# Kernel tuning notes

Measured on AMD Instinct MI355X. Metric: run time of the kernel, lower is better.

Reference implementation:

```python
import jax, jax.numpy as jnp
import numpy as np

N = 50000
E = 800000
IN_C = 1024
HID = 64
HEADS = 4
OUT_C = 64
NEG_SLOPE = 0.2  # PyG GATConv default


def setup_inputs() -> dict:
    key = jax.random.key(0)
    ks = jax.random.split(key, 12)
    x = jax.random.normal(ks[0], (N, IN_C), dtype=jnp.float32)
    edge_index = jax.random.randint(ks[1], (2, E), 0, N, dtype=jnp.int64)
    s1 = 1.0 / np.sqrt(IN_C)
    s2 = 1.0 / np.sqrt(HEADS * HID)
    return {
        "x": x,
        "edge_index": edge_index,
        "W1": jax.random.normal(ks[2], (HEADS * HID, IN_C), dtype=jnp.float32) * s1,
        "a_src1": jax.random.normal(ks[3], (HEADS, HID), dtype=jnp.float32) * s2,
        "a_dst1": jax.random.normal(ks[4], (HEADS, HID), dtype=jnp.float32) * s2,
        "b1": jnp.zeros((HEADS * HID,), dtype=jnp.float32),
        "W2": jax.random.normal(ks[5], (OUT_C, HEADS * HID), dtype=jnp.float32) * s2,
        "a_src2": jax.random.normal(ks[6], (1, OUT_C), dtype=jnp.float32) * 0.1,
        "a_dst2": jax.random.normal(ks[7], (1, OUT_C), dtype=jnp.float32) * 0.1,
        "b2": jnp.zeros((OUT_C,), dtype=jnp.float32),
    }


def gat_conv(x, src, dst, W, a_src, a_dst, b, heads, concat):
    # x: [N, F_in]; src/dst: [E'] (self-loops already appended)
    n = x.shape[0]
    h = (x @ W.T).reshape(n, heads, -1)                 # [N, H, C]
    alpha_s = (h * a_src).sum(-1)                       # [N, H]
    alpha_d = (h * a_dst).sum(-1)                       # [N, H]
    e = jax.nn.leaky_relu(alpha_s[src] + alpha_d[dst], NEG_SLOPE)  # [E', H]
    # segment softmax over edges grouped by destination
    m = jax.ops.segment_max(e, dst, num_segments=n)     # [N, H]
    ex = jnp.exp(e - m[dst])
    denom = jax.ops.segment_sum(ex, dst, num_segments=n)
    alpha = ex / denom[dst]                             # [E', H]
    out = jax.ops.segment_sum(alpha[:, :, None] * h[src], dst, num_segments=n)  # [N, H, C]
    out = out.reshape(n, -1) if concat else out.mean(axis=1)
    return out + b


def reference(x, edge_index, W1, a_src1, a_dst1, b1, W2, a_src2, a_dst2, b2):
    n = x.shape[0]
    loop = jnp.arange(n, dtype=edge_index.dtype)
    src = jnp.concatenate([edge_index[0], loop])  # PyG add_self_loops=True
    dst = jnp.concatenate([edge_index[1], loop])
    # eval mode: dropout is identity
    h = gat_conv(x, src, dst, W1, a_src1, a_dst1, b1, HEADS, concat=True)
    h = jax.nn.elu(h)
    out = gat_conv(h, src, dst, W2, a_src2, a_dst2, b2, 1, concat=False)
    return out
```

## Files before the change

kernel.cpp:

```cpp
#include <hip/hip_runtime.h>
#include <hip/hip_bf16.h>
#include <math.h>

constexpr int IN_C = 1024;
constexpr int HEADS = 4;
constexpr int F1 = 256;
constexpr int OUT_C = 64;
constexpr float NEG = 0.2f;

using bf16x8 = __attribute__((ext_vector_type(8))) short;
using f32x4 = __attribute__((ext_vector_type(4))) float;

__device__ __forceinline__ float leaky(float x) { return x > 0.f ? x : NEG * x; }

__device__ __forceinline__ unsigned short bf16bits(float v) {
  __hip_bfloat16 b = __float2bfloat16(v);
  return *reinterpret_cast<unsigned short*>(&b);
}
__device__ __forceinline__ float bf2f(unsigned short u) {
  union { unsigned u; float f; } c; c.u = (unsigned)u << 16; return c.f;
}

#define GLD_LDS16(g, l)                                                        \
  __builtin_amdgcn_global_load_lds(                                            \
      (const __attribute__((address_space(1))) void*)(g),                      \
      (__attribute__((address_space(3))) void*)(l), 16, 0, 0)

constexpr int NB_W1 = (F1 * IN_C) / 256;
constexpr int NB_W2 = (OUT_C * F1) / 256;

__global__ __launch_bounds__(256) void prep_kernel(const float* __restrict__ W1,
                                                   unsigned short* __restrict__ W1b,
                                                   const float* __restrict__ W2,
                                                   unsigned short* __restrict__ W2b,
                                                   const int* __restrict__ ei, int E, int N,
                                                   int* __restrict__ deg) {
  int b = blockIdx.x;
  if (b < NB_W1) {
    int i = b * 256 + threadIdx.x;
    W1b[i] = bf16bits(W1[i]);
  } else if (b < NB_W1 + NB_W2) {
    int i = (b - NB_W1) * 256 + threadIdx.x;
    W2b[i] = bf16bits(W2[i]);
  } else {
    int e = (b - NB_W1 - NB_W2) * 256 + threadIdx.x;
    if (e < E + N) {
      int dst = (e < E) ? ei[E + e] : (e - E);
      atomicAdd(&deg[dst], 1);
    }
  }
}

constexpr int LDTA = 72;

__global__ __launch_bounds__(256, 3) void gemm1_mfma(const float* __restrict__ X,
                                                     const unsigned short* __restrict__ Wb,
                                                     unsigned short* __restrict__ Hb,
                                                     const float* __restrict__ a_src,
                                                     const float* __restrict__ a_dst,
                                                     float* __restrict__ as_out,
                                                     float* __restrict__ ad_out, int M, int MB,
                                                     const int* __restrict__ ei, int E, int N,
                                                     const int* __restrict__ row_ptr,
                                                     int* __restrict__ fill,
                                                     int* __restrict__ col) {
  __shared__ unsigned short As[64 * LDTA];
  __shared__ unsigned short Bs[256 * 64];
  const int tid = threadIdx.x;

  if (blockIdx.x >= MB) {
    int e = (blockIdx.x - MB) * 256 + tid;
    int ET = E + N;
    if (e < ET) {
      int src, dst;
      if (e < E) { src = ei[e]; dst = ei[E + e]; }
      else       { src = e - E; dst = e - E; }
      int pos = row_ptr[dst] + atomicAdd(&fill[dst], 1);
      col[pos] = src;
    }
    return;
  }

  const int wave = tid >> 6;
  const int lane = tid & 63;
  const int m15 = lane & 15;
  const int q = lane >> 4;
  const int bm = blockIdx.x * 64;

  f32x4 acc[4][4];
#pragma unroll
  for (int i = 0; i < 4; ++i)
#pragma unroll
    for (int j = 0; j < 4; ++j) acc[i][j] = (f32x4){0.f, 0.f, 0.f, 0.f};

  const int ar = tid >> 2;
  const int acg = (tid & 3) * 16;
  const int agr = (bm + ar < M) ? (bm + ar) : (M - 1);
  const float* aptr = X + (size_t)agr * IN_C + acg;

  float4 a0 = *(const float4*)(aptr + 0);
  float4 a1 = *(const float4*)(aptr + 4);
  float4 a2 = *(const float4*)(aptr + 8);
  float4 a3 = *(const float4*)(aptr + 12);

  for (int kt = 0; kt < IN_C; kt += 64) {
#pragma unroll
    for (int p = 0; p < 8; ++p) {
      int s = p * 256 + tid;
      int r = s >> 3;
      int cb = s & 7;
      const unsigned short* g = Wb + (size_t)r * IN_C + kt + ((cb ^ (r & 7)) << 3);
      GLD_LDS16(g, &Bs[(p * 256 + wave * 64) * 8]);
    }
    union { uint4 u4[2]; __hip_bfloat162 h[8]; } pk;
    pk.h[0] = __float22bfloat162_rn(make_float2(a0.x, a0.y));
    pk.h[1] = __float22bfloat162_rn(make_float2(a0.z, a0.w));
    pk.h[2] = __float22bfloat162_rn(make_float2(a1.x, a1.y));
    pk.h[3] = __float22bfloat162_rn(make_float2(a1.z, a1.w));
    pk.h[4] = __float22bfloat162_rn(make_float2(a2.x, a2.y));
    pk.h[5] = __float22bfloat162_rn(make_float2(a2.z, a2.w));
    pk.h[6] = __float22bfloat162_rn(make_float2(a3.x, a3.y));
    pk.h[7] = __float22bfloat162_rn(make_float2(a3.z, a3.w));
    *(uint4*)&As[ar * LDTA + acg] = pk.u4[0];
    *(uint4*)&As[ar * LDTA + acg + 8] = pk.u4[1];
    if (kt + 64 < IN_C) {
      a0 = *(const float4*)(aptr + kt + 64 + 0);
      a1 = *(const float4*)(aptr + kt + 64 + 4);
      a2 = *(const float4*)(aptr + kt + 64 + 8);
      a3 = *(const float4*)(aptr + kt + 64 + 12);
    }
    __syncthreads();

#pragma unroll
    for (int k0 = 0; k0 < 64; k0 += 32) {
      bf16x8 af[4], bfr[4];
#pragma unroll
      for (int i = 0; i < 4; ++i)
        af[i] = *(const bf16x8*)&As[(i * 16 + m15) * LDTA + k0 + q * 8];
#pragma unroll
      for (int j = 0; j < 4; ++j) {
        int rb = wave * 64 + j * 16 + m15;
        int cbp = ((k0 >> 3) + q) ^ (rb & 7);
        bfr[j] = *(const bf16x8*)&Bs[rb * 64 + cbp * 8];
      }
#pragma unroll
      for (int i = 0; i < 4; ++i)
#pragma unroll
        for (int j = 0; j < 4; ++j)
          acc[i][j] = __builtin_amdgcn_mfma_f32_16x16x32_bf16(af[i], bfr[j], acc[i][j], 0, 0, 0);
    }
    __syncthreads();
  }
  float asf[4], adf[4];
#pragma unroll
  for (int j = 0; j < 4; ++j) {
    asf[j] = a_src[wave * 64 + j * 16 + m15];
    adf[j] = a_dst[wave * 64 + j * 16 + m15];
  }
#pragma unroll
  for (int i = 0; i < 4; ++i) {
#pragma unroll
    for (int r = 0; r < 4; ++r) {
      int row = bm + i * 16 + q * 4 + r;
      if (row < M) {
#pragma unroll
        for (int j = 0; j < 4; ++j)
          Hb[(size_t)row * F1 + wave * 64 + j * 16 + m15] = bf16bits(acc[i][j][r]);
      }
      float s = acc[i][0][r] * asf[0] + acc[i][1][r] * asf[1] +
                acc[i][2][r] * asf[2] + acc[i][3][r] * asf[3];
      float d = acc[i][0][r] * adf[0] + acc[i][1][r] * adf[1] +
                acc[i][2][r] * adf[2] + acc[i][3][r] * adf[3];
#pragma unroll
      for (int o = 1; o < 16; o <<= 1) {
        s += __shfl_xor(s, o, 64);
        d += __shfl_xor(d, o, 64);
      }
      if (m15 == 0 && row < M) {
        as_out[row * HEADS + wave] = s;
        ad_out[row * HEADS + wave] = d;
      }
    }
  }
}

__global__ __launch_bounds__(256, 4) void gemm2_mfma(const unsigned short* __restrict__ Y,
                                                     const unsigned short* __restrict__ W2b,
                                                     float* __restrict__ H2,
                                                     const float* __restrict__ a_src,
                                                     const float* __restrict__ a_dst,
                                                     float* __restrict__ as_out,
                                                     float* __restrict__ ad_out, int M) {
  __shared__ unsigned short As[64 * 64];
  __shared__ unsigned short Bs[64 * 64];
  const int tid = threadIdx.x;
  const int wave = tid >> 6;
  const int lane = tid & 63;
  const int m15 = lane & 15;
  const int q = lane >> 4;
  const int bm = blockIdx.x * 64;

  f32x4 acc[4];
#pragma unroll
  for (int j = 0; j < 4; ++j) acc[j] = (f32x4){0.f, 0.f, 0.f, 0.f};

  for (int kt = 0; kt < F1; kt += 64) {
#pragma unroll
    for (int p = 0; p < 2; ++p) {
      int s = p * 256 + tid;
      int r = s >> 3;
      int cb = s & 7;
      int colo = (cb ^ (r & 7)) << 3;
      int gr = (bm + r < M) ? (bm + r) : (M - 1);
      GLD_LDS16(Y + (size_t)gr * F1 + kt + colo, &As[(p * 256 + wave * 64) * 8]);
      GLD_LDS16(W2b + (size_t)r * F1 + kt + colo, &Bs[(p * 256 + wave * 64) * 8]);
    }
    __syncthreads();
#pragma unroll
    for (int k0 = 0; k0 < 64; k0 += 32) {
      int ra = wave * 16 + m15;
      bf16x8 af = *(const bf16x8*)&As[ra * 64 + ((((k0 >> 3) + q) ^ (ra & 7)) << 3)];
      bf16x8 bfr[4];
#pragma unroll
      for (int j = 0; j < 4; ++j) {
        int rb = j * 16 + m15;
        bfr[j] = *(const bf16x8*)&Bs[rb * 64 + ((((k0 >> 3) + q) ^ (rb & 7)) << 3)];
      }
#pragma unroll
      for (int j = 0; j < 4; ++j)
        acc[j] = __builtin_amdgcn_mfma_f32_16x16x32_bf16(af, bfr[j], acc[j], 0, 0, 0);
    }
    __syncthreads();
  }
  float asf[4], adf[4];
#pragma unroll
  for (int j = 0; j < 4; ++j) {
    asf[j] = a_src[j * 16 + m15];
    adf[j] = a_dst[j * 16 + m15];
  }
#pragma unroll
  for (int r = 0; r < 4; ++r) {
    int row = bm + wave * 16 + q * 4 + r;
    if (row < M) {
#pragma unroll
      for (int j = 0; j < 4; ++j) H2[(size_t)row * OUT_C + j * 16 + m15] = acc[j][r];
    }
    float s = acc[0][r] * asf[0] + acc[1][r] * asf[1] + acc[2][r] * asf[2] + acc[3][r] * asf[3];
    float d = acc[0][r] * adf[0] + acc[1][r] * adf[1] + acc[2][r] * adf[2] + acc[3][r] * adf[3];
#pragma unroll
    for (int o = 1; o < 16; o <<= 1) {
      s += __shfl_xor(s, o, 64);
      d += __shfl_xor(d, o, 64);
    }
    if (m15 == 0 && row < M) {
      as_out[row] = s;
      ad_out[row] = d;
    }
  }
}

__global__ __launch_bounds__(256) void scan_block_sums(const int* __restrict__ deg,
                                                       int* __restrict__ part, int n) {
  __shared__ int sm[256];
  int t = threadIdx.x;
  int i = blockIdx.x * 256 + t;
  sm[t] = (i < n) ? deg[i] : 0;
  __syncthreads();
  for (int off = 128; off > 0; off >>= 1) {
    if (t < off) sm[t] += sm[t + off];
    __syncthreads();
  }
  if (t == 0) part[blockIdx.x] = sm[0];
}

__global__ __launch_bounds__(256) void scan_final2(const int* __restrict__ deg,
                                                   const int* __restrict__ part,
                                                   int* __restrict__ row_ptr, int n) {
  __shared__ int sm[256];
  __shared__ int wsum[4];
  int t = threadIdx.x;
  int i = blockIdx.x * 256 + t;
  sm[t] = (i < n) ? deg[i] : 0;
  int pv = (t < blockIdx.x) ? part[t] : 0;
#pragma unroll
  for (int o = 1; o < 64; o <<= 1) pv += __shfl_xor(pv, o, 64);
  if ((t & 63) == 0) wsum[t >> 6] = pv;
  __syncthreads();
  for (int off = 1; off < 256; off <<= 1) {
    int u = (t >= off) ? sm[t - off] : 0;
    __syncthreads();
    sm[t] += u;
    __syncthreads();
  }
  int base = wsum[0] + wsum[1] + wsum[2] + wsum[3];
  if (i < n) row_ptr[i + 1] = base + sm[t];
  if (i == 0) row_ptr[0] = 0;
}

__global__ __launch_bounds__(256) void agg1_kernel(const unsigned short* __restrict__ hb,
                                                   const float* __restrict__ as,
                                                   const float* __restrict__ ad,
                                                   const int* __restrict__ row_ptr,
                                                   const int* __restrict__ col,
                                                   const float* __restrict__ bias,
                                                   unsigned short* __restrict__ yb, int N) {
  int dst = (blockIdx.x * blockDim.x + threadIdx.x) >> 6;
  int lane = threadIdx.x & 63;
  if (dst >= N) return;
  const int s0 = row_ptr[dst], s1 = row_ptr[dst + 1];
  const int par = lane >> 5;
  const int cg = lane & 31;
  const int hh = cg >> 3;
  const float adl = ad[dst * 4 + hh];
  float acc[8];
#pragma unroll
  for (int k = 0; k < 8; ++k) acc[k] = 0.f;
  float den = 0.f;

  int i = s0 + par;
  for (; i + 6 < s1; i += 8) {
    int sA = col[i], sB = col[i + 2], sC = col[i + 4], sD = col[i + 6];
    float wA = __expf(leaky(as[sA * 4 + hh] + adl));
    float wB = __expf(leaky(as[sB * 4 + hh] + adl));
    float wC = __expf(leaky(as[sC * 4 + hh] + adl));
    float wD = __expf(leaky(as[sD * 4 + hh] + adl));
    uint4 hA = *(const uint4*)(hb + (size_t)sA * F1 + cg * 8);
    uint4 hB = *(const uint4*)(hb + (size_t)sB * F1 + cg * 8);
    uint4 hC = *(const uint4*)(hb + (size_t)sC * F1 + cg * 8);
    uint4 hD = *(const uint4*)(hb + (size_t)sD * F1 + cg * 8);
    den += (wA + wB) + (wC + wD);
    const unsigned short* pa = (const unsigned short*)&hA;
    const unsigned short* pb = (const unsigned short*)&hB;
    const unsigned short* pc = (const unsigned short*)&hC;
    const unsigned short* pd = (const unsigned short*)&hD;
#pragma unroll
    for (int k = 0; k < 8; ++k) {
      acc[k] = fmaf(wA, bf2f(pa[k]), acc[k]);
      acc[k] = fmaf(wB, bf2f(pb[k]), acc[k]);
      acc[k] = fmaf(wC, bf2f(pc[k]), acc[k]);
      acc[k] = fmaf(wD, bf2f(pd[k]), acc[k]);
    }
  }
  for (; i + 2 < s1; i += 4) {
    int sA = col[i], sB = col[i + 2];
    float wA = __expf(leaky(as[sA * 4 + hh] + adl));
    float wB = __expf(leaky(as[sB * 4 + hh] + adl));
    uint4 hA = *(const uint4*)(hb + (size_t)sA * F1 + cg * 8);
    uint4 hB = *(const uint4*)(hb + (size_t)sB * F1 + cg * 8);
    den += wA + wB;
    const unsigned short* pa = (const unsigned short*)&hA;
    const unsigned short* pb = (const unsigned short*)&hB;
#pragma unroll
    for (int k = 0; k < 8; ++k) {
      acc[k] = fmaf(wA, bf2f(pa[k]), acc[k]);
      acc[k] = fmaf(wB, bf2f(pb[k]), acc[k]);
    }
  }
  for (; i < s1; i += 2) {
    int s = col[i];
    float w = __expf(leaky(as[s * 4 + hh] + adl));
    uint4 hv = *(const uint4*)(hb + (size_t)s * F1 + cg * 8);
    den += w;
    const unsigned short* p = (const unsigned short*)&hv;
#pragma unroll
    for (int k = 0; k < 8; ++k) acc[k] = fmaf(w, bf2f(p[k]), acc[k]);
  }
  den += __shfl_xor(den, 32, 64);
#pragma unroll
  for (int k = 0; k < 8; ++k) acc[k] += __shfl_xor(acc[k], 32, 64);

  if (par == 0) {
    const float iv = 1.f / den;
    float4 b0 = *(const float4*)(bias + cg * 8);
    float4 b1 = *(const float4*)(bias + cg * 8 + 4);
    float bv[8] = {b0.x, b0.y, b0.z, b0.w, b1.x, b1.y, b1.z, b1.w};
    ushort4 o[2];
    unsigned short* po = (unsigned short*)o;
#pragma unroll
    for (int k = 0; k < 8; ++k) {
      float v = acc[k] * iv + bv[k];
      v = v > 0.f ? v : (__expf(v) - 1.f);
      po[k] = bf16bits(v);
    }
    *(uint4*)(yb + (size_t)dst * F1 + cg * 8) = *(uint4*)o;
  }
}

__global__ __launch_bounds__(256) void agg2_kernel(const float* __restrict__ h,
                                                   const float* __restrict__ as,
                                                   const float* __restrict__ ad,
                                                   const int* __restrict__ row_ptr,
                                                   const int* __restrict__ col,
                                                   const float* __restrict__ bias,
                                                   float* __restrict__ out, int N) {
  int dst = (blockIdx.x * blockDim.x + threadIdx.x) >> 6;
  int lane = threadIdx.x & 63;
  if (dst >= N) return;
  const int s0 = row_ptr[dst], s1 = row_ptr[dst + 1];
  const int par = lane >> 5;
  const int cg = lane & 31;
  const float adl = ad[dst];
  float a0 = 0.f, a1 = 0.f, den = 0.f;

  int i = s0 + par;
  for (; i + 6 < s1; i += 8) {
    int sA = col[i], sB = col[i + 2], sC = col[i + 4], sD = col[i + 6];
    float wA = __expf(leaky(as[sA] + adl));
    float wB = __expf(leaky(as[sB] + adl));
    float wC = __expf(leaky(as[sC] + adl));
    float wD = __expf(leaky(as[sD] + adl));
    float2 hA = *(const float2*)(h + (size_t)sA * OUT_C + cg * 2);
    float2 hB = *(const float2*)(h + (size_t)sB * OUT_C + cg * 2);
    float2 hC = *(const float2*)(h + (size_t)sC * OUT_C + cg * 2);
    float2 hD = *(const float2*)(h + (size_t)sD * OUT_C + cg * 2);
    den += (wA + wB) + (wC + wD);
    a0 = fmaf(wA, hA.x, a0); a1 = fmaf(wA, hA.y, a1);
    a0 = fmaf(wB, hB.x, a0); a1 = fmaf(wB, hB.y, a1);
    a0 = fmaf(wC, hC.x, a0); a1 = fmaf(wC, hC.y, a1);
    a0 = fmaf(wD, hD.x, a0); a1 = fmaf(wD, hD.y, a1);
  }
  for (; i + 2 < s1; i += 4) {
    int sA = col[i], sB = col[i + 2];
    float wA = __expf(leaky(as[sA] + adl));
    float wB = __expf(leaky(as[sB] + adl));
    float2 hA = *(const float2*)(h + (size_t)sA * OUT_C + cg * 2);
    float2 hB = *(const float2*)(h + (size_t)sB * OUT_C + cg * 2);
    den += wA + wB;
    a0 = fmaf(wA, hA.x, a0); a1 = fmaf(wA, hA.y, a1);
    a0 = fmaf(wB, hB.x, a0); a1 = fmaf(wB, hB.y, a1);
  }
  for (; i < s1; i += 2) {
    int s = col[i];
    float w = __expf(leaky(as[s] + adl));
    float2 hv = *(const float2*)(h + (size_t)s * OUT_C + cg * 2);
    den += w;
    a0 = fmaf(w, hv.x, a0); a1 = fmaf(w, hv.y, a1);
  }
  den += __shfl_xor(den, 32, 64);
  a0 += __shfl_xor(a0, 32, 64);
  a1 += __shfl_xor(a1, 32, 64);
  if (par == 0) {
    const float iv = 1.f / den;
    float2 bv = *(const float2*)(bias + cg * 2);
    float2 o = make_float2(a0 * iv + bv.x, a1 * iv + bv.y);
    *(float2*)(out + (size_t)dst * OUT_C + cg * 2) = o;
  }
}

extern "C" void kernel_launch(void* const* d_in, const int* in_sizes, int n_in,
                              void* d_out, int out_size, void* d_ws, size_t ws_size,
                              hipStream_t stream) {
  const float* x      = (const float*)d_in[0];
  const int*   ei     = (const int*)d_in[1];
  const float* W1     = (const float*)d_in[2];
  const float* a_src1 = (const float*)d_in[3];
  const float* a_dst1 = (const float*)d_in[4];
  const float* b1     = (const float*)d_in[5];
  const float* W2     = (const float*)d_in[6];
  const float* a_src2 = (const float*)d_in[7];
  const float* a_dst2 = (const float*)d_in[8];
  const float* b2     = (const float*)d_in[9];
  float* out = (float*)d_out;

  const int N = in_sizes[0] / IN_C;
  const int E = in_sizes[1] / 2;
  const int ET = E + N;

  char* ws = (char*)d_ws;
  size_t off = 0;
  auto alloc = [&](size_t bytes) -> void* {
    void* p = ws + off;
    off = (off + bytes + 255) & ~(size_t)255;
    return p;
  };
  unsigned short* h1b = (unsigned short*)alloc((size_t)N * F1 * 2);
  unsigned short* y1b = (unsigned short*)alloc((size_t)N * F1 * 2);
  float* h2      = (float*)alloc((size_t)N * OUT_C * 4);
  float* as1     = (float*)alloc((size_t)N * HEADS * 4);
  float* ad1     = (float*)alloc((size_t)N * HEADS * 4);
  float* as2     = (float*)alloc((size_t)N * 4);
  float* ad2     = (float*)alloc((size_t)N * 4);
  int*   deg     = (int*)alloc((size_t)N * 2 * 4);
  int*   fill    = deg + N;
  int*   row_ptr = (int*)alloc((size_t)(N + 1) * 4);
  int*   col     = (int*)alloc((size_t)ET * 4);
  int*   part    = (int*)alloc(1024 * 4);
  unsigned short* W1b = (unsigned short*)alloc((size_t)F1 * IN_C * 2);
  unsigned short* W2b = (unsigned short*)alloc((size_t)OUT_C * F1 * 2);
  (void)off; (void)ws_size; (void)n_in; (void)out_size;

  hipMemsetAsync(deg, 0, (size_t)N * 2 * 4, stream);

  const int NBD = (ET + 255) / 256;
  const int P = (N + 255) / 256;

  prep_kernel<<<NB_W1 + NB_W2 + NBD, 256, 0, stream>>>(W1, W1b, W2, W2b, ei, E, N, deg);
  scan_block_sums<<<P, 256, 0, stream>>>(deg, part, N);
  scan_final2<<<P, 256, 0, stream>>>(deg, part, row_ptr, N);

  const int NB4 = (N + 3) / 4;
  const int MB = (N + 63) / 64;
  const int SB = (ET + 255) / 256;

  gemm1_mfma<<<MB + SB, 256, 0, stream>>>(x, W1b, h1b, a_src1, a_dst1, as1, ad1, N, MB,
                                          ei, E, N, row_ptr, fill, col);
  agg1_kernel<<<NB4, 256, 0, stream>>>(h1b, as1, ad1, row_ptr, col, b1, y1b, N);

  gemm2_mfma<<<(N + 63) / 64, 256, 0, stream>>>(y1b, W2b, h2, a_src2, a_dst2, as2, ad2, N);
  agg2_kernel<<<NB4, 256, 0, stream>>>(h2, as2, ad2, row_ptr, col, b2, out, N);
}
```

Baseline: 515.6 us.

## Retile gemm1 to 128x128 blocks with direct-to-LDS fp32 X loads and swizzle

Measured after the change: 504.3 us. 1.02x faster.

```diff
diff --git a/kernel.cpp b/kernel.cpp
--- a/kernel.cpp
+++ b/kernel.cpp
@@ -51,25 +51,23 @@
   }
 }
 
-constexpr int LDTA = 72;
-
 __global__ __launch_bounds__(256, 3) void gemm1_mfma(const float* __restrict__ X,
                                                      const unsigned short* __restrict__ Wb,
                                                      unsigned short* __restrict__ Hb,
                                                      const float* __restrict__ a_src,
                                                      const float* __restrict__ a_dst,
                                                      float* __restrict__ as_out,
-                                                     float* __restrict__ ad_out, int M, int MB,
+                                                     float* __restrict__ ad_out, int M, int MB2,
                                                      const int* __restrict__ ei, int E, int N,
                                                      const int* __restrict__ row_ptr,
                                                      int* __restrict__ fill,
                                                      int* __restrict__ col) {
-  __shared__ unsigned short As[64 * LDTA];
-  __shared__ unsigned short Bs[256 * 64];
+  __shared__ float As4[128 * 64];
+  __shared__ unsigned short Bs[128 * 64];
   const int tid = threadIdx.x;
 
-  if (blockIdx.x >= MB) {
-    int e = (blockIdx.x - MB) * 256 + tid;
+  if (blockIdx.x >= MB2) {
+    int e = (blockIdx.x - MB2) * 256 + tid;
     int ET = E + N;
     if (e < ET) {
       int src, dst;
@@ -81,53 +79,39 @@
     return;
   }
 
+  const int rc = blockIdx.x >> 1;
+  const int colg = blockIdx.x & 1;
   const int wave = tid >> 6;
+  const int rg = wave >> 1;
+  const int cg = wave & 1;
   const int lane = tid & 63;
   const int m15 = lane & 15;
   const int q = lane >> 4;
-  const int bm = blockIdx.x * 64;
+  const int bm = rc * 128;
 
   f32x4 acc[4][4];
 #pragma unroll
   for (int i = 0; i < 4; ++i)
 #pragma unroll
     for (int j = 0; j < 4; ++j) acc[i][j] = (f32x4){0.f, 0.f, 0.f, 0.f};
-
-  const int ar = tid >> 2;
-  const int acg = (tid & 3) * 16;
-  const int agr = (bm + ar < M) ? (bm + ar) : (M - 1);
-  const float* aptr = X + (size_t)agr * IN_C + acg;
-
-  float4 a0 = *(const float4*)(aptr + 0);
-  float4 a1 = *(const float4*)(aptr + 4);
-  float4 a2 = *(const float4*)(aptr + 8);
-  float4 a3 = *(const float4*)(aptr + 12);
 
   for (int kt = 0; kt < IN_C; kt += 64) {
 #pragma unroll
     for (int p = 0; p < 8; ++p) {
       int s = p * 256 + tid;
-      int r = s >> 3;
-      int cb = s & 7;
-      const unsigned short* g = Wb + (size_t)r * IN_C + kt + ((cb ^ (r & 7)) << 3);
-      GLD_LDS16(g, &Bs[(p * 256 + wave * 64) * 8]);
-    }
-    union { uint4 u4[2]; __hip_bfloat162 h[8]; } pk;
-    pk.h[0] = __float22bfloat162_rn(make_float2(a0.x, a0.y));
-    pk.h[1] = __float22bfloat162_rn(make_float2(a0.z, a0.w));
-    pk.h[2] = __float22bfloat162_rn(make_float2(a1.x, a1.y));
-    pk.h[3] = __float22bfloat162_rn(make_float2(a1.z, a1.w));
-    pk.h[4] = __float22bfloat162_rn(make_float2(a2.x, a2.y));
-    pk.h[5] = __float22bfloat162_rn(make_float2(a2.z, a2.w));
-    pk.h[6] = __float22bfloat162_rn(make_float2(a3.x, a3.y));
-    pk.h[7] = __float22bfloat162_rn(make_float2(a3.z, a3.w));
-    *(uint4*)&As[ar * LDTA + acg] = pk.u4[0];
-    *(uint4*)&As[ar * LDTA + acg + 8] = pk.u4[1];
-    if (kt + 64 < IN_C) {
-      a0 = *(const float4*)(aptr + kt + 64 + 0);
-      a1 = *(const float4*)(aptr + kt + 64 + 4);
-      a2 = *(const float4*)(aptr + kt + 64 + 8);
-      a3 = *(const float4*)(aptr + kt + 64 + 12);
+      int r = s >> 4;
+      int cb = s & 15;
+      int gr = (bm + r < M) ? (bm + r) : (M - 1);
+      const float* g = X + (size_t)gr * IN_C + kt + ((cb ^ (r & 15)) << 2);
+      GLD_LDS16(g, &As4[s * 4]);
+    }
+#pragma unroll
+    for (int p = 0; p < 4; ++p) {
+      int t = p * 256 + tid;
+      int rB = t >> 3;
+      int cbB = t & 7;
+      const unsigned short* g = Wb + (size_t)(colg * 128 + rB) * IN_C + kt + ((cbB ^ (rB & 7)) << 3);
+      GLD_LDS16(g, &Bs[t * 8]);
     }
     __syncthreads();
 
@@ -135,11 +119,21 @@
     for (int k0 = 0; k0 < 64; k0 += 32) {
       bf16x8 af[4], bfr[4];
 #pragma unroll
-      for (int i = 0; i < 4; ++i)
-        af[i] = *(const bf16x8*)&As[(i * 16 + m15) * LDTA + k0 + q * 8];
+      for (int i = 0; i < 4; ++i) {
+        int ra = rg * 64 + i * 16 + m15;
+        int c0 = (k0 >> 2) + q * 2;
+        float4 f0 = *(const float4*)&As4[ra * 64 + ((c0 ^ (ra & 15)) << 2)];
+        float4 f1 = *(const float4*)&As4[ra * 64 + (((c0 + 1) ^ (ra & 15)) << 2)];
+        union { bf16x8 v; __hip_bfloat162 h[4]; } pk;
+        pk.h[0] = __float22bfloat162_rn(make_float2(f0.x, f0.y));
+        pk.h[1] = __float22bfloat162_rn(make_float2(f0.z, f0.w));
+        pk.h[2] = __float22bfloat162_rn(make_float2(f1.x, f1.y));
+        pk.h[3] = __float22bfloat162_rn(make_float2(f1.z, f1.w));
+        af[i] = pk.v;
+      }
 #pragma unroll
       for (int j = 0; j < 4; ++j) {
-        int rb = wave * 64 + j * 16 + m15;
+        int rb = cg * 64 + j * 16 + m15;
         int cbp = ((k0 >> 3) + q) ^ (rb & 7);
         bfr[j] = *(const bf16x8*)&Bs[rb * 64 + cbp * 8];
       }
@@ -151,21 +145,24 @@
     }
     __syncthreads();
   }
+
+  const int cbase = colg * 128 + cg * 64;
+  const int head = colg * 2 + cg;
   float asf[4], adf[4];
 #pragma unroll
   for (int j = 0; j < 4; ++j) {
-    asf[j] = a_src[wave * 64 + j * 16 + m15];
-    adf[j] = a_dst[wave * 64 + j * 16 + m15];
+    asf[j] = a_src[cbase + j * 16 + m15];
+    adf[j] = a_dst[cbase + j * 16 + m15];
   }
 #pragma unroll
   for (int i = 0; i < 4; ++i) {
 #pragma unroll
     for (int r = 0; r < 4; ++r) {
-      int row = bm + i * 16 + q * 4 + r;
+      int row = bm + rg * 64 + i * 16 + q * 4 + r;
       if (row < M) {
 #pragma unroll
         for (int j = 0; j < 4; ++j)
-          Hb[(size_t)row * F1 + wave * 64 + j * 16 + m15] = bf16bits(acc[i][j][r]);
+          Hb[(size_t)row * F1 + cbase + j * 16 + m15] = bf16bits(acc[i][j][r]);
       }
       float s = acc[i][0][r] * asf[0] + acc[i][1][r] * asf[1] +
                 acc[i][2][r] * asf[2] + acc[i][3][r] * asf[3];
@@ -177,8 +174,8 @@
         d += __shfl_xor(d, o, 64);
       }
       if (m15 == 0 && row < M) {
-        as_out[row * HEADS + wave] = s;
-        ad_out[row * HEADS + wave] = d;
+        as_out[row * HEADS + head] = s;
+        ad_out[row * HEADS + head] = d;
       }
     }
   }
@@ -499,11 +496,11 @@
   scan_final2<<<P, 256, 0, stream>>>(deg, part, row_ptr, N);
 
   const int NB4 = (N + 3) / 4;
-  const int MB = (N + 63) / 64;
+  const int MB2 = ((N + 127) / 128) * 2;
   const int SB = (ET + 255) / 256;
 
-  gemm1_mfma<<<MB + SB, 256, 0, stream>>>(x, W1b, h1b, a_src1, a_dst1, as1, ad1, N, MB,
-                                          ei, E, N, row_ptr, fill, col);
+  gemm1_mfma<<<MB2 + SB, 256, 0, stream>>>(x, W1b, h1b, a_src1, a_dst1, as1, ad1, N, MB2,
+                                           ei, E, N, row_ptr, fill, col);
   agg1_kernel<<<NB4, 256, 0, stream>>>(h1b, as1, ad1, row_ptr, col, b1, y1b, N);
 
   gemm2_mfma<<<(N + 63) / 64, 256, 0, stream>>>(y1b, W2b, h2, a_src2, a_dst2, as2, ad2, N);
```
